# Kernel optimization log

Hardware: AMD Instinct MI355X
Metric: run time of the kernel (lower is better)

Reference implementation:

```python
import jax, jax.numpy as jnp
import numpy as np

B, T, H, STEPS = 8192, 128, 128, 30
BN_EPS = 1e-5


def gru_cell(x, h, w_ih, w_hh, b_ih, b_hh):
    # PyTorch GRU gate math: gates ordered (r, z, n)
    gi = x @ w_ih.T + b_ih            # [B, 3H]
    gh = h @ w_hh.T + b_hh            # [B, 3H]
    ir, iz, inn = jnp.split(gi, 3, axis=-1)
    hr, hz, hn = jnp.split(gh, 3, axis=-1)
    r = jax.nn.sigmoid(ir + hr)
    z = jax.nn.sigmoid(iz + hz)
    n = jnp.tanh(inn + r * hn)
    return (1.0 - z) * n + z * h


def setup_inputs() -> dict:
    key = jax.random.key(0)
    ks = jax.random.split(key, 10)
    s = lambda k, shape: jax.random.normal(k, shape, jnp.float32) * 0.05
    z = lambda *shape: jnp.zeros(shape, jnp.float32)
    return {
        "past": jax.random.normal(ks[0], (B, 6, T), jnp.float32),
        "conv_w": s(ks[1], (H, 6, 3)),
        "conv_b": z(H),
        "bn_gamma": jnp.ones((1,), jnp.float32),
        "bn_beta": z(1),
        "bn_mean": z(1),
        "bn_var": jnp.ones((1,), jnp.float32),
        "enc_wih": s(ks[2], (3 * H, H)),
        "enc_whh": s(ks[3], (3 * H, H)),
        "enc_bih": z(3 * H),
        "enc_bhh": z(3 * H),
        "dec_wih": s(ks[4], (3 * H, H)),
        "dec_whh": s(ks[5], (3 * H, H)),
        "dec_bih": z(3 * H),
        "dec_bhh": z(3 * H),
        "fc1_w": s(ks[6], (256, H)),
        "fc1_b": z(256),
        "fc2_w": s(ks[7], (64, 256)),
        "fc2_b": z(64),
        "fc3_w": s(ks[8], (6, 64)),
        "fc3_b": z(6),
    }


def reference(past, conv_w, conv_b, bn_gamma, bn_beta, bn_mean, bn_var,
              enc_wih, enc_whh, enc_bih, enc_bhh,
              dec_wih, dec_whh, dec_bih, dec_bhh,
              fc1_w, fc1_b, fc2_w, fc2_b, fc3_w, fc3_b):
    b = past.shape[0]
    # Conv1d(6 -> 128, k=3, pad=1) + ReLU
    y = jax.lax.conv_general_dilated(
        past, conv_w, window_strides=(1,), padding=[(1, 1)],
        dimension_numbers=("NCH", "OIH", "NCH"))
    y = jax.nn.relu(y + conv_b[None, :, None])
    # BatchNorm2d(1) in eval mode: single-channel affine normalization over whole tensor
    y = bn_gamma[0] * (y - bn_mean[0]) * jax.lax.rsqrt(bn_var[0] + BN_EPS) + bn_beta[0]
    # encoder GRU over time: [B,128,T] -> [T,B,128]
    xs = jnp.transpose(y, (2, 0, 1))
    h0 = jnp.zeros((b, H), y.dtype)

    def enc_step(h, x):
        return gru_cell(x, h, enc_wih, enc_whh, enc_bih, enc_bhh), None

    state_past, _ = jax.lax.scan(enc_step, h0, xs)  # [B,128]

    def mlp(h):
        a = jax.nn.relu(h @ fc1_w.T + fc1_b)
        a = a @ fc2_w.T + fc2_b   # no activation between fc2 and fc3 (matches Sequential)
        return a @ fc3_w.T + fc3_b

    # decoder input is state_past at step 0, zeros afterwards
    dec_inputs = jnp.concatenate(
        [state_past[None], jnp.zeros((STEPS - 1, b, H), y.dtype)], axis=0)
    present0 = past[:, :, -1]  # [B,6]

    def dec_step(carry, x):
        h, present = carry
        h = gru_cell(x, h, dec_wih, dec_whh, dec_bih, dec_bhh)
        present = present + mlp(h)
        return (h, present), present

    _, preds = jax.lax.scan(dec_step, (jnp.zeros((b, H), y.dtype), present0), dec_inputs)
    # preds: [30,B,6] -> [B,6,30] (matches prediction.permute(0,2,1))
    return jnp.transpose(preds, (1, 2, 0))
```

## Files before the change

### kernel.cpp

```cpp
#include <hip/hip_runtime.h>

#define DI __device__ __forceinline__

typedef __attribute__((ext_vector_type(8))) short short8;
typedef __attribute__((ext_vector_type(4))) float f32x4;

constexpr int THREADS = 512;
constexpr int ROWS    = 32;
constexpr int NBLK    = 8192 / ROWS;
constexpr int PITCH   = 272;
constexpr int PITCH2  = 528;
constexpr int SPITCH  = 256;

constexpr int O_STAGE = 0;
constexpr int O_PATCH = 98304;
constexpr int O_XALL  = 108544;
constexpr int O_H     = 143360;
constexpr int HBUF    = 8704;
constexpr int O_FC3W  = 160768;
constexpr int LDS_TOTAL = 162304;
constexpr int O_A1D   = 98304;
constexpr int O_A2D   = 115200;

DI unsigned cvtpk2(float lo, float hi){
  unsigned r;
  asm("v_cvt_pk_bf16_f32 %0, %1, %2" : "=v"(r) : "v"(lo), "v"(hi));
  return r;
}
DI unsigned short f2bf(float f){ return (unsigned short)cvtpk2(f, f); }
DI float bf2f(unsigned short u){
  union { unsigned u; float f; } v; v.u = ((unsigned)u) << 16;
  return v.f;
}
DI float u2f_lo(unsigned u){ union { unsigned u; float f; } v; v.u = u << 16;        return v.f; }
DI float u2f_hi(unsigned u){ union { unsigned u; float f; } v; v.u = u & 0xffff0000u; return v.f; }
DI float sigm(float x){ return __builtin_amdgcn_rcpf(1.f + __expf(-x)); }
DI float tanh_(float x){ return 2.f * __builtin_amdgcn_rcpf(1.f + __expf(-2.f * x)) - 1.f; }
DI f32x4 mfma16(short8 a, short8 b, f32x4 c){
  return __builtin_amdgcn_mfma_f32_16x16x32_bf16(a, b, c, 0, 0, 0);
}
DI uint2 pack4(f32x4 v){
  return make_uint2(cvtpk2(v[0], v[1]), cvtpk2(v[2], v[3]));
}
DI f32x4 unpack4(uint2 u){
  return (f32x4){u2f_lo(u.x), u2f_hi(u.x), u2f_lo(u.y), u2f_hi(u.y)};
}

DI void stage_k128(char* dst, const float* __restrict__ src, int nrows, int tid){
  const int total = nrows * 32;
  for (int i = tid; i < total; i += THREADS){
    float4 v = ((const float4*)src)[i];
    int e = i << 2;
    int n = e >> 7, k = e & 127;
    *(uint2*)(dst + n * SPITCH + k * 2) = make_uint2(cvtpk2(v.x, v.y), cvtpk2(v.z, v.w));
  }
}
DI void stage_k256(char* dst, const float* __restrict__ src, int nrows, int tid){
  const int total = nrows * 64;
  for (int i = tid; i < total; i += THREADS){
    float4 v = ((const float4*)src)[i];
    int e = i << 2;
    int n = e >> 8, k = e & 255;
    *(uint2*)(dst + n * PITCH2 + k * 2) = make_uint2(cvtpk2(v.x, v.y), cvtpk2(v.z, v.w));
  }
}

__global__ void __launch_bounds__(THREADS, 2)
gru_fused(const float* __restrict__ past,
          const float* __restrict__ conv_w, const float* __restrict__ conv_b,
          const float* __restrict__ bn_gamma, const float* __restrict__ bn_beta,
          const float* __restrict__ bn_mean, const float* __restrict__ bn_var,
          const float* __restrict__ enc_wih, const float* __restrict__ enc_whh,
          const float* __restrict__ enc_bih, const float* __restrict__ enc_bhh,
          const float* __restrict__ dec_wih, const float* __restrict__ dec_whh,
          const float* __restrict__ dec_bih, const float* __restrict__ dec_bhh,
          const float* __restrict__ fc1_w, const float* __restrict__ fc1_b,
          const float* __restrict__ fc2_w, const float* __restrict__ fc2_b,
          const float* __restrict__ fc3_w, const float* __restrict__ fc3_b,
          float* __restrict__ out)
{
  extern __shared__ char smem[];
  const int tid  = threadIdx.x;
  const int lane = tid & 63, w = tid >> 6;
  const int l15  = lane & 15, quad = lane >> 4;
  const int b0   = blockIdx.x * ROWS;
  const int col  = w * 16 + l15;

  const float br_e  = enc_bih[col]       + enc_bhh[col];
  const float bz_e  = enc_bih[128 + col] + enc_bhh[128 + col];
  const float bin_e = enc_bih[256 + col];
  const float bhn_e = enc_bhh[256 + col];
  const float br_d  = dec_bih[col]       + dec_bhh[col];
  const float bz_d  = dec_bih[128 + col] + dec_bhh[128 + col];
  const float bin_d = dec_bih[256 + col];
  const float bhn_d = dec_bhh[256 + col];
  const float cb_t  = conv_b[col];
  const float s_bn  = bn_gamma[0] * rsqrtf(bn_var[0] + 1e-5f);
  const float o_bn  = bn_beta[0] - bn_mean[0] * s_bn;
  const float fb1a  = fc1_b[w * 32 + l15];
  const float fb1b  = fc1_b[w * 32 + 16 + l15];
  const int   mt2   = w & 1, nt2 = w >> 1;
  const float fb2   = fc2_b[nt2 * 16 + l15];

  for (int i = tid; i < 2*HBUF/4; i += THREADS) ((unsigned*)(smem + O_H))[i] = 0u;

  short8 wf[3][4], wh[3][4];
  stage_k128(smem + O_STAGE, enc_wih, 384, tid);
  __syncthreads();
  #pragma unroll
  for (int g = 0; g < 3; ++g)
    #pragma unroll
    for (int kt = 0; kt < 4; ++kt)
      wf[g][kt] = *(const short8*)(smem + O_STAGE + (g*128 + col)*SPITCH + kt*64 + quad*16);
  __syncthreads();
  stage_k128(smem + O_STAGE, enc_whh, 384, tid);
  __syncthreads();
  #pragma unroll
  for (int g = 0; g < 3; ++g)
    #pragma unroll
    for (int kt = 0; kt < 4; ++kt)
      wh[g][kt] = *(const short8*)(smem + O_STAGE + (g*128 + col)*SPITCH + kt*64 + quad*16);
  __syncthreads();

  for (int i = tid; i < 2560; i += THREADS) ((unsigned*)(smem + O_STAGE))[i] = 0u;
  __syncthreads();
  for (int i = tid; i < 2304; i += THREADS){
    int oc = i / 18, kk = i - oc * 18;
    *(unsigned short*)(smem + O_STAGE + oc*80 + kk*2) = f2bf(conv_w[i]);
  }
  __syncthreads();
  const short8 cwf = *(const short8*)(smem + O_STAGE + col*80 + quad*16);
  __syncthreads();

  for (int i = tid; i < 12672; i += THREADS) ((unsigned*)(smem + O_STAGE))[i] = 0u;
  __syncthreads();
  for (int i4 = tid; i4 < 6144; i4 += THREADS){
    int m = i4 / 192, rem = i4 - m*192, c = rem >> 5, t4 = (rem & 31) << 2;
    float4 v = *(const float4*)(past + (size_t)(b0 + m)*768 + c*128 + t4);
    unsigned short* dst = (unsigned short*)(smem + O_STAGE + ((m*6 + c)*132 + t4 + 1)*2);
    dst[0] = f2bf(v.x); dst[1] = f2bf(v.y); dst[2] = f2bf(v.z); dst[3] = f2bf(v.w);
  }
  for (int i = tid; i < 384; i += THREADS) ((float*)(smem + O_FC3W))[i] = fc3_w[i];
  __syncthreads();

  const int e0 = tid;
  const int m0 = e0 / 18, r0 = e0 - m0*18, c0 = r0 / 3, k0 = r0 - c0*3;
  const int e1 = tid + 512;
  const int m1 = e1 / 18, r1 = e1 - m1*18, c1 = r1 / 3, k1 = r1 - c1*3;

  auto patch_entry = [&](int t0, int m, int r18, int c, int k){
    int base = (m*6 + c)*132 + t0 + k;
    const unsigned* pl = (const unsigned*)(smem + O_STAGE);
    unsigned w0 = pl[base >> 1], w1 = pl[(base >> 1) + 1], w2 = pl[(base >> 1) + 2];
    int sh = (base & 1) * 16;
    unsigned long long lo = (unsigned long long)w0 | ((unsigned long long)w1 << 32);
    unsigned long long hi = (unsigned long long)w1 | ((unsigned long long)w2 << 32);
    unsigned a01 = (unsigned)(lo >> sh);
    unsigned a23 = (unsigned)(hi >> sh);
    char* pb = smem + O_PATCH + m*80 + r18*2;
    *(unsigned short*)(pb)          = (unsigned short)(a01 & 0xffff);
    *(unsigned short*)(pb + 2560)   = (unsigned short)(a01 >> 16);
    *(unsigned short*)(pb + 5120)   = (unsigned short)(a23 & 0xffff);
    *(unsigned short*)(pb + 7680)   = (unsigned short)(a23 >> 16);
  };
  auto patchA1 = [&](int t0){
    patch_entry(t0, m0, r0, c0, k0);
    if (e1 < 576) patch_entry(t0, m1, r1, c1, k1);
  };

  uint2 gi_pk[4][2][3];
  float hreg[8];
  #pragma unroll
  for (int i = 0; i < 8; ++i) hreg[i] = 0.f;

  auto conv_block = [&](){
    #pragma unroll
    for (int mt8 = 0; mt8 < 8; ++mt8){
      short8 pa = *(const short8*)(smem + O_PATCH + (mt8*16 + l15)*80 + quad*16);
      f32x4 cc = (f32x4){0.f,0.f,0.f,0.f};
      cc = mfma16(pa, cwf, cc);
      #pragma unroll
      for (int r = 0; r < 4; ++r){
        int mrow = mt8*16 + quad*4 + r;
        float vx = s_bn * fmaxf(cc[r] + cb_t, 0.f) + o_bn;
        *(unsigned short*)(smem + O_XALL + mrow*PITCH + col*2) = f2bf(vx);
      }
    }
  };
  auto gi_unit = [&](int tc, int mt){
    short8 a[4];
    #pragma unroll
    for (int kt = 0; kt < 4; ++kt)
      a[kt] = *(const short8*)(smem + O_XALL + ((tc*2 + mt)*16 + l15)*PITCH + kt*64 + quad*16);
    f32x4 g0 = (f32x4){0.f,0.f,0.f,0.f}, g1 = g0, g2 = g0;
    #pragma unroll
    for (int kt = 0; kt < 4; ++kt){
      g0 = mfma16(a[kt], wf[0][kt], g0);
      g1 = mfma16(a[kt], wf[1][kt], g1);
      g2 = mfma16(a[kt], wf[2][kt], g2);
    }
    gi_pk[tc][mt][0] = pack4(g0);
    gi_pk[tc][mt][1] = pack4(g1);
    gi_pk[tc][mt][2] = pack4(g2);
  };
  auto step_body = [&](int t){
    const int tc = t & 3;
    const char* hr = smem + O_H + (t & 1) * HBUF;
    char*       hw = smem + O_H + ((t + 1) & 1) * HBUF;
    f32x4 accr[2], accz[2], accn2[2], gin[2];
    #pragma unroll
    for (int mt = 0; mt < 2; ++mt){
      accr[mt]  = unpack4(gi_pk[tc][mt][0]);
      accz[mt]  = unpack4(gi_pk[tc][mt][1]);
      gin[mt]   = unpack4(gi_pk[tc][mt][2]);
      accn2[mt] = (f32x4){0.f,0.f,0.f,0.f};
    }
    short8 ha[2][4];
    #pragma unroll
    for (int mt = 0; mt < 2; ++mt)
      #pragma unroll
      for (int kt = 0; kt < 4; ++kt)
        ha[mt][kt] = *(const short8*)(hr + (mt*16 + l15)*PITCH + kt*64 + quad*16);
    #pragma unroll
    for (int mt = 0; mt < 2; ++mt)
      #pragma unroll
      for (int kt = 0; kt < 4; ++kt){
        accr[mt]  = mfma16(ha[mt][kt], wh[0][kt], accr[mt]);
        accz[mt]  = mfma16(ha[mt][kt], wh[1][kt], accz[mt]);
        accn2[mt] = mfma16(ha[mt][kt], wh[2][kt], accn2[mt]);
      }
    #pragma unroll
    for (int mt = 0; mt < 2; ++mt)
      #pragma unroll
      for (int r = 0; r < 4; ++r){
        float rg = sigm(accr[mt][r] + br_e);
        float zg = sigm(accz[mt][r] + bz_e);
        float ng = tanh_(gin[mt][r] + bin_e + rg*(accn2[mt][r] + bhn_e));
        hreg[mt*4 + r] = ng + zg*(hreg[mt*4 + r] - ng);
      }
    #pragma unroll
    for (int mt = 0; mt < 2; ++mt)
      #pragma unroll
      for (int r = 0; r < 4; ++r)
        *(unsigned short*)(hw + (mt*16 + quad*4 + r)*PITCH + col*2) = f2bf(hreg[mt*4 + r]);
  };

  patchA1(0);
  __syncthreads();
  conv_block();
  __syncthreads();
  #pragma unroll
  for (int tc = 0; tc < 4; ++tc){ gi_unit(tc, 0); gi_unit(tc, 1); }
  patchA1(4);
  __syncthreads();

  for (int c = 0; c < 32; ++c){
    const int t0 = c * 4;
    const bool prod = (c < 31);
    step_body(t0 + 0);
    if (prod) conv_block();
    __syncthreads();
    step_body(t0 + 1);
    if (prod){ gi_unit(0,0); gi_unit(0,1); gi_unit(1,0); }
    __syncthreads();
    step_body(t0 + 2);
    if (prod){ gi_unit(1,1); gi_unit(2,0); gi_unit(2,1); }
    __syncthreads();
    step_body(t0 + 3);
    if (prod){ gi_unit(3,0); gi_unit(3,1); if (c < 30) patchA1(t0 + 8); }
    __syncthreads();
  }

  stage_k128(smem + O_STAGE, dec_wih, 384, tid);
  __syncthreads();
  #pragma unroll
  for (int g = 0; g < 3; ++g)
    #pragma unroll
    for (int kt = 0; kt < 4; ++kt)
      wf[g][kt] = *(const short8*)(smem + O_STAGE + (g*128 + col)*SPITCH + kt*64 + quad*16);
  f32x4 gi0r[2], gi0z[2], gi0n[2];
  {
    short8 hea[2][4];
    #pragma unroll
    for (int mt = 0; mt < 2; ++mt)
      #pragma unroll
      for (int kt = 0; kt < 4; ++kt)
        hea[mt][kt] = *(const short8*)(smem + O_H + (mt*16 + l15)*PITCH + kt*64 + quad*16);
    #pragma unroll
    for (int mt = 0; mt < 2; ++mt){
      gi0r[mt] = (f32x4){0.f,0.f,0.f,0.f}; gi0z[mt] = gi0r[mt]; gi0n[mt] = gi0r[mt];
      #pragma unroll
      for (int kt = 0; kt < 4; ++kt){
        gi0r[mt] = mfma16(hea[mt][kt], wf[0][kt], gi0r[mt]);
        gi0z[mt] = mfma16(hea[mt][kt], wf[1][kt], gi0z[mt]);
        gi0n[mt] = mfma16(hea[mt][kt], wf[2][kt], gi0n[mt]);
      }
    }
  }
  __syncthreads();
  stage_k128(smem + O_STAGE, dec_whh, 384, tid);
  __syncthreads();
  #pragma unroll
  for (int g = 0; g < 3; ++g)
    #pragma unroll
    for (int kt = 0; kt < 4; ++kt)
      wh[g][kt] = *(const short8*)(smem + O_STAGE + (g*128 + col)*SPITCH + kt*64 + quad*16);
  __syncthreads();
  short8 f1f[2][4], f2f[8];
  stage_k128(smem + O_STAGE, fc1_w, 256, tid);
  __syncthreads();
  #pragma unroll
  for (int j = 0; j < 2; ++j)
    #pragma unroll
    for (int kt = 0; kt < 4; ++kt)
      f1f[j][kt] = *(const short8*)(smem + O_STAGE + (w*32 + j*16 + l15)*SPITCH + kt*64 + quad*16);
  __syncthreads();
  stage_k256(smem + O_STAGE, fc2_w, 64, tid);
  __syncthreads();
  #pragma unroll
  for (int kt = 0; kt < 8; ++kt)
    f2f[kt] = *(const short8*)(smem + O_STAGE + (nt2*16 + l15)*PITCH2 + kt*64 + quad*16);
  __syncthreads();
  for (int i = tid; i < HBUF/4; i += THREADS) ((unsigned*)(smem + O_H + HBUF))[i] = 0u;
  #pragma unroll
  for (int i = 0; i < 8; ++i) hreg[i] = 0.f;
  const int prow = tid / 6, pcol = tid - prow*6;
  float present = 0.f, fb3 = 0.f;
  if (tid < 192){
    present = past[(size_t)(b0 + prow)*768 + pcol*128 + 127];
    fb3 = fc3_b[pcol];
  }
  __syncthreads();

  for (int s = 0; s < 30; ++s){
    const char* hr = smem + O_H + (1 - (s & 1)) * HBUF;
    char*       hw = smem + O_H + (s & 1) * HBUF;
    f32x4 accr[2], accz[2], accn2[2], gin[2];
    #pragma unroll
    for (int mt = 0; mt < 2; ++mt){
      if (s == 0){ accr[mt] = gi0r[mt]; accz[mt] = gi0z[mt]; gin[mt] = gi0n[mt]; }
      else       { accr[mt] = (f32x4){0.f,0.f,0.f,0.f}; accz[mt] = accr[mt]; gin[mt] = accr[mt]; }
      accn2[mt] = (f32x4){0.f,0.f,0.f,0.f};
    }
    {
      short8 ha[2][4];
      #pragma unroll
      for (int mt = 0; mt < 2; ++mt)
        #pragma unroll
        for (int kt = 0; kt < 4; ++kt)
          ha[mt][kt] = *(const short8*)(hr + (mt*16 + l15)*PITCH + kt*64 + quad*16);
      #pragma unroll
      for (int mt = 0; mt < 2; ++mt)
        #pragma unroll
        for (int kt = 0; kt < 4; ++kt){
          accr[mt]  = mfma16(ha[mt][kt], wh[0][kt], accr[mt]);
          accz[mt]  = mfma16(ha[mt][kt], wh[1][kt], accz[mt]);
          accn2[mt] = mfma16(ha[mt][kt], wh[2][kt], accn2[mt]);
        }
    }
    #pragma unroll
    for (int mt = 0; mt < 2; ++mt)
      #pragma unroll
      for (int r = 0; r < 4; ++r){
        float rg = sigm(accr[mt][r] + br_d);
        float zg = sigm(accz[mt][r] + bz_d);
        float ng = tanh_(gin[mt][r] + bin_d + rg*(accn2[mt][r] + bhn_d));
        hreg[mt*4 + r] = ng + zg*(hreg[mt*4 + r] - ng);
      }
    #pragma unroll
    for (int mt = 0; mt < 2; ++mt)
      #pragma unroll
      for (int r = 0; r < 4; ++r)
        *(unsigned short*)(hw + (mt*16 + quad*4 + r)*PITCH + col*2) = f2bf(hreg[mt*4 + r]);
    __syncthreads();

    {
      short8 hf[2][4];
      #pragma unroll
      for (int mt = 0; mt < 2; ++mt)
        #pragma unroll
        for (int kt = 0; kt < 4; ++kt)
          hf[mt][kt] = *(const short8*)(hw + (mt*16 + l15)*PITCH + kt*64 + quad*16);
      f32x4 a1a[2][2];
      #pragma unroll
      for (int mt = 0; mt < 2; ++mt)
        #pragma unroll
        for (int j = 0; j < 2; ++j) a1a[mt][j] = (f32x4){0.f,0.f,0.f,0.f};
      #pragma unroll
      for (int j = 0; j < 2; ++j)
        #pragma unroll
        for (int kt = 0; kt < 4; ++kt){
          a1a[0][j] = mfma16(hf[0][kt], f1f[j][kt], a1a[0][j]);
          a1a[1][j] = mfma16(hf[1][kt], f1f[j][kt], a1a[1][j]);
        }
      #pragma unroll
      for (int mt = 0; mt < 2; ++mt)
        #pragma unroll
        for (int j = 0; j < 2; ++j){
          float bb = j ? fb1b : fb1a;
          #pragma unroll
          for (int r = 0; r < 4; ++r)
            *(unsigned short*)(smem + O_A1D + (mt*16 + quad*4 + r)*PITCH2 +
                               (w*32 + j*16 + l15)*2) = f2bf(fmaxf(a1a[mt][j][r] + bb, 0.f));
        }
    }
    __syncthreads();

    {
      f32x4 a2a = (f32x4){0.f,0.f,0.f,0.f};
      #pragma unroll
      for (int kt = 0; kt < 8; ++kt){
        short8 a = *(const short8*)(smem + O_A1D + (mt2*16 + l15)*PITCH2 + kt*64 + quad*16);
        a2a = mfma16(a, f2f[kt], a2a);
      }
      #pragma unroll
      for (int r = 0; r < 4; ++r)
        *(unsigned short*)(smem + O_A2D + (mt2*16 + quad*4 + r)*144 + (nt2*16 + l15)*2) =
            f2bf(a2a[r] + fb2);
    }
    __syncthreads();

    if (tid < 192){
      float o = fb3;
      const float* w3 = (const float*)(smem + O_FC3W) + pcol*64;
      #pragma unroll
      for (int kc = 0; kc < 8; ++kc){
        short8 av = *(const short8*)(smem + O_A2D + prow*144 + kc*16);
        #pragma unroll
        for (int j = 0; j < 8; ++j)
          o += bf2f((unsigned short)av[j]) * w3[kc*8 + j];
      }
      present += o;
      out[(size_t)(b0 + prow)*180 + pcol*30 + s] = present;
    }
  }
}

extern "C" void kernel_launch(void* const* d_in, const int* in_sizes, int n_in,
                              void* d_out, int out_size, void* d_ws, size_t ws_size,
                              hipStream_t stream) {
  (void)in_sizes; (void)n_in; (void)out_size; (void)d_ws; (void)ws_size;
  const float* past     = (const float*)d_in[0];
  const float* conv_w   = (const float*)d_in[1];
  const float* conv_b   = (const float*)d_in[2];
  const float* bn_gamma = (const float*)d_in[3];
  const float* bn_beta  = (const float*)d_in[4];
  const float* bn_mean  = (const float*)d_in[5];
  const float* bn_var   = (const float*)d_in[6];
  const float* enc_wih  = (const float*)d_in[7];
  const float* enc_whh  = (const float*)d_in[8];
  const float* enc_bih  = (const float*)d_in[9];
  const float* enc_bhh  = (const float*)d_in[10];
  const float* dec_wih  = (const float*)d_in[11];
  const float* dec_whh  = (const float*)d_in[12];
  const float* dec_bih  = (const float*)d_in[13];
  const float* dec_bhh  = (const float*)d_in[14];
  const float* fc1_w    = (const float*)d_in[15];
  const float* fc1_b    = (const float*)d_in[16];
  const float* fc2_w    = (const float*)d_in[17];
  const float* fc2_b    = (const float*)d_in[18];
  const float* fc3_w    = (const float*)d_in[19];
  const float* fc3_b    = (const float*)d_in[20];

  hipFuncSetAttribute((const void*)gru_fused,
                      hipFuncAttributeMaxDynamicSharedMemorySize, LDS_TOTAL);

  gru_fused<<<NBLK, THREADS, LDS_TOTAL, stream>>>(
      past, conv_w, conv_b, bn_gamma, bn_beta, bn_mean, bn_var,
      enc_wih, enc_whh, enc_bih, enc_bhh,
      dec_wih, dec_whh, dec_bih, dec_bhh,
      fc1_w, fc1_b, fc2_w, fc2_b, fc3_w, fc3_b,
      (float*)d_out);
}
```

Before: 471.9 us.

## Fold fc2 into fc3 algebraically and keep encoder input gates in fp32

fc2 and fc3 are linear with nothing between them, so the change precomputes W3·W2 (6x256) and the combined bias once per block in LDS. Each decoder step then does a single MFMA pass over the fc1 activations instead of fc2 MFMA, a barrier, and a scalar fc3 dot product. This removes one __syncthreads and the A2D round trip per step. Separately, the encoder's precomputed input-gate tiles are now held as fp32 registers instead of packed bf16, which drops the pack/unpack work but raises register pressure under launch bounds of 2 blocks per CU.

```diff
diff --git a/kernel.cpp b/kernel.cpp
--- a/kernel.cpp
+++ b/kernel.cpp
@@ -20,7 +20,8 @@
 constexpr int O_FC3W  = 160768;
 constexpr int LDS_TOTAL = 162304;
 constexpr int O_A1D   = 98304;
-constexpr int O_A2D   = 115200;
+constexpr int O_W32   = 115200;
+constexpr int O_B32   = 123648;
 
 DI unsigned cvtpk2(float lo, float hi){
   unsigned r;
@@ -32,18 +33,10 @@
   union { unsigned u; float f; } v; v.u = ((unsigned)u) << 16;
   return v.f;
 }
-DI float u2f_lo(unsigned u){ union { unsigned u; float f; } v; v.u = u << 16;        return v.f; }
-DI float u2f_hi(unsigned u){ union { unsigned u; float f; } v; v.u = u & 0xffff0000u; return v.f; }
 DI float sigm(float x){ return __builtin_amdgcn_rcpf(1.f + __expf(-x)); }
 DI float tanh_(float x){ return 2.f * __builtin_amdgcn_rcpf(1.f + __expf(-2.f * x)) - 1.f; }
 DI f32x4 mfma16(short8 a, short8 b, f32x4 c){
   return __builtin_amdgcn_mfma_f32_16x16x32_bf16(a, b, c, 0, 0, 0);
-}
-DI uint2 pack4(f32x4 v){
-  return make_uint2(cvtpk2(v[0], v[1]), cvtpk2(v[2], v[3]));
-}
-DI f32x4 unpack4(uint2 u){
-  return (f32x4){u2f_lo(u.x), u2f_hi(u.x), u2f_lo(u.y), u2f_hi(u.y)};
 }
 
 DI void stage_k128(char* dst, const float* __restrict__ src, int nrows, int tid){
@@ -53,15 +46,6 @@
     int e = i << 2;
     int n = e >> 7, k = e & 127;
     *(uint2*)(dst + n * SPITCH + k * 2) = make_uint2(cvtpk2(v.x, v.y), cvtpk2(v.z, v.w));
-  }
-}
-DI void stage_k256(char* dst, const float* __restrict__ src, int nrows, int tid){
-  const int total = nrows * 64;
-  for (int i = tid; i < total; i += THREADS){
-    float4 v = ((const float4*)src)[i];
-    int e = i << 2;
-    int n = e >> 8, k = e & 255;
-    *(uint2*)(dst + n * PITCH2 + k * 2) = make_uint2(cvtpk2(v.x, v.y), cvtpk2(v.z, v.w));
   }
 }
 
@@ -99,8 +83,6 @@
   const float o_bn  = bn_beta[0] - bn_mean[0] * s_bn;
   const float fb1a  = fc1_b[w * 32 + l15];
   const float fb1b  = fc1_b[w * 32 + 16 + l15];
-  const int   mt2   = w & 1, nt2 = w >> 1;
-  const float fb2   = fc2_b[nt2 * 16 + l15];
 
   for (int i = tid; i < 2*HBUF/4; i += THREADS) ((unsigned*)(smem + O_H))[i] = 0u;
 
@@ -168,7 +150,7 @@
     if (e1 < 576) patch_entry(t0, m1, r1, c1, k1);
   };
 
-  uint2 gi_pk[4][2][3];
+  f32x4 gi_f[4][2][3];
   float hreg[8];
   #pragma unroll
   for (int i = 0; i < 8; ++i) hreg[i] = 0.f;
@@ -199,20 +181,19 @@
       g1 = mfma16(a[kt], wf[1][kt], g1);
       g2 = mfma16(a[kt], wf[2][kt], g2);
     }
-    gi_pk[tc][mt][0] = pack4(g0);
-    gi_pk[tc][mt][1] = pack4(g1);
-    gi_pk[tc][mt][2] = pack4(g2);
+    gi_f[tc][mt][0] = g0;
+    gi_f[tc][mt][1] = g1;
+    gi_f[tc][mt][2] = g2;
   };
-  auto step_body = [&](int t){
-    const int tc = t & 3;
+  auto step_body = [&](int t, int tc){
     const char* hr = smem + O_H + (t & 1) * HBUF;
     char*       hw = smem + O_H + ((t + 1) & 1) * HBUF;
     f32x4 accr[2], accz[2], accn2[2], gin[2];
     #pragma unroll
     for (int mt = 0; mt < 2; ++mt){
-      accr[mt]  = unpack4(gi_pk[tc][mt][0]);
-      accz[mt]  = unpack4(gi_pk[tc][mt][1]);
-      gin[mt]   = unpack4(gi_pk[tc][mt][2]);
+      accr[mt]  = gi_f[tc][mt][0];
+      accz[mt]  = gi_f[tc][mt][1];
+      gin[mt]   = gi_f[tc][mt][2];
       accn2[mt] = (f32x4){0.f,0.f,0.f,0.f};
     }
     short8 ha[2][4];
@@ -257,16 +238,16 @@
   for (int c = 0; c < 32; ++c){
     const int t0 = c * 4;
     const bool prod = (c < 31);
-    step_body(t0 + 0);
+    step_body(t0 + 0, 0);
     if (prod) conv_block();
     __syncthreads();
-    step_body(t0 + 1);
+    step_body(t0 + 1, 1);
     if (prod){ gi_unit(0,0); gi_unit(0,1); gi_unit(1,0); }
     __syncthreads();
-    step_body(t0 + 2);
+    step_body(t0 + 2, 2);
     if (prod){ gi_unit(1,1); gi_unit(2,0); gi_unit(2,1); }
     __syncthreads();
-    step_body(t0 + 3);
+    step_body(t0 + 3, 3);
     if (prod){ gi_unit(3,0); gi_unit(3,1); if (c < 30) patchA1(t0 + 8); }
     __syncthreads();
   }
@@ -306,7 +287,7 @@
     for (int kt = 0; kt < 4; ++kt)
       wh[g][kt] = *(const short8*)(smem + O_STAGE + (g*128 + col)*SPITCH + kt*64 + quad*16);
   __syncthreads();
-  short8 f1f[2][4], f2f[8];
+  short8 f1f[2][4];
   stage_k128(smem + O_STAGE, fc1_w, 256, tid);
   __syncthreads();
   #pragma unroll
@@ -315,22 +296,40 @@
     for (int kt = 0; kt < 4; ++kt)
       f1f[j][kt] = *(const short8*)(smem + O_STAGE + (w*32 + j*16 + l15)*SPITCH + kt*64 + quad*16);
   __syncthreads();
-  stage_k256(smem + O_STAGE, fc2_w, 64, tid);
-  __syncthreads();
-  #pragma unroll
-  for (int kt = 0; kt < 8; ++kt)
-    f2f[kt] = *(const short8*)(smem + O_STAGE + (nt2*16 + l15)*PITCH2 + kt*64 + quad*16);
-  __syncthreads();
+
+  for (int i = tid; i < 2112; i += THREADS) ((unsigned*)(smem + O_W32))[i] = 0u;
+  __syncthreads();
+  {
+    const int kk = tid & 255, wn = (tid >> 8) * 3;
+    const float* f3p = (const float*)(smem + O_FC3W);
+    float o0 = 0.f, o1 = 0.f, o2 = 0.f;
+    for (int j = 0; j < 64; ++j){
+      float cv = fc2_w[j*256 + kk];
+      o0 += f3p[(wn+0)*64 + j] * cv;
+      o1 += f3p[(wn+1)*64 + j] * cv;
+      o2 += f3p[(wn+2)*64 + j] * cv;
+    }
+    *(unsigned short*)(smem + O_W32 + (wn+0)*PITCH2 + kk*2) = f2bf(o0);
+    *(unsigned short*)(smem + O_W32 + (wn+1)*PITCH2 + kk*2) = f2bf(o1);
+    *(unsigned short*)(smem + O_W32 + (wn+2)*PITCH2 + kk*2) = f2bf(o2);
+    if (tid < 6){
+      float ob = fc3_b[tid];
+      for (int j = 0; j < 64; ++j) ob += f3p[tid*64 + j] * fc2_b[j];
+      ((float*)(smem + O_B32))[tid] = ob;
+    }
+  }
   for (int i = tid; i < HBUF/4; i += THREADS) ((unsigned*)(smem + O_H + HBUF))[i] = 0u;
   #pragma unroll
   for (int i = 0; i < 8; ++i) hreg[i] = 0.f;
-  const int prow = tid / 6, pcol = tid - prow*6;
-  float present = 0.f, fb3 = 0.f;
-  if (tid < 192){
-    present = past[(size_t)(b0 + prow)*768 + pcol*128 + 127];
-    fb3 = fc3_b[pcol];
-  }
-  __syncthreads();
+  __syncthreads();
+  float pres[4] = {0.f, 0.f, 0.f, 0.f};
+  float b32v = 0.f;
+  if (w < 2 && l15 < 6){
+    b32v = ((const float*)(smem + O_B32))[l15];
+    #pragma unroll
+    for (int r = 0; r < 4; ++r)
+      pres[r] = past[(size_t)(b0 + w*16 + quad*4 + r)*768 + l15*128 + 127];
+  }
 
   for (int s = 0; s < 30; ++s){
     const char* hr = smem + O_H + (1 - (s & 1)) * HBUF;
@@ -406,32 +405,21 @@
     }
     __syncthreads();
 
-    {
-      f32x4 a2a = (f32x4){0.f,0.f,0.f,0.f};
+    if (w < 2){
+      f32x4 acc = (f32x4){0.f,0.f,0.f,0.f};
       #pragma unroll
       for (int kt = 0; kt < 8; ++kt){
-        short8 a = *(const short8*)(smem + O_A1D + (mt2*16 + l15)*PITCH2 + kt*64 + quad*16);
-        a2a = mfma16(a, f2f[kt], a2a);
-      }
-      #pragma unroll
-      for (int r = 0; r < 4; ++r)
-        *(unsigned short*)(smem + O_A2D + (mt2*16 + quad*4 + r)*144 + (nt2*16 + l15)*2) =
-            f2bf(a2a[r] + fb2);
-    }
-    __syncthreads();
-
-    if (tid < 192){
-      float o = fb3;
-      const float* w3 = (const float*)(smem + O_FC3W) + pcol*64;
-      #pragma unroll
-      for (int kc = 0; kc < 8; ++kc){
-        short8 av = *(const short8*)(smem + O_A2D + prow*144 + kc*16);
-        #pragma unroll
-        for (int j = 0; j < 8; ++j)
-          o += bf2f((unsigned short)av[j]) * w3[kc*8 + j];
-      }
-      present += o;
-      out[(size_t)(b0 + prow)*180 + pcol*30 + s] = present;
+        short8 a   = *(const short8*)(smem + O_A1D + (w*16 + l15)*PITCH2 + kt*64 + quad*16);
+        short8 bfr = *(const short8*)(smem + O_W32 + l15*PITCH2 + kt*64 + quad*16);
+        acc = mfma16(a, bfr, acc);
+      }
+      if (l15 < 6){
+        #pragma unroll
+        for (int r = 0; r < 4; ++r){
+          pres[r] += acc[r] + b32v;
+          out[(size_t)(b0 + w*16 + quad*4 + r)*180 + l15*30 + s] = pres[r];
+        }
+      }
     }
   }
 }
```

Result: no change. 465.8 us (-1.3%).
